# Kernel optimization log

Hardware: AMD Instinct MI355X
Metric: run time of the kernel (lower is better)

Reference implementation:

```python
import jax, jax.numpy as jnp
import numpy as np

B, H, S, D = 2, 16, 2048, 64
NUM_EMB = 8192  # 2 * max_position_embeddings


def setup_inputs() -> dict:
    key = jax.random.key(0)
    k1, k2, k3 = jax.random.split(key, 3)
    query = jax.random.normal(k1, (B, H, S, D), dtype=jnp.float32)
    attention_scores = jax.random.normal(k2, (B, H, S, S), dtype=jnp.float32)
    rel_emb = jax.random.normal(k3, (NUM_EMB, D), dtype=jnp.float32)
    return {"query": query, "attention_scores": attention_scores, "rel_emb": rel_emb}


def reference(query, attention_scores, rel_emb):
    seq_len = query.shape[2]
    pos = jnp.arange(seq_len)
    # relative ids in [0, 2*max_pos): (j - i) + num_embeddings // 2
    rel_ids = pos[None, :] - pos[:, None] + rel_emb.shape[0] // 2  # [S, S]
    bias = rel_emb[rel_ids]  # [S, S, D] gather (Toeplitz structure)
    # rel_logits[b,h,i,j] = sum_d query[b,h,i,d] * bias[i,j,d]
    rel_logits = jnp.einsum('bhid,ijd->bhij', query, bias)
    return attention_scores + rel_logits
```

## Files before the change

kernel.cpp:

```cpp
#include <hip/hip_runtime.h>

#define BH     32
#define S_LEN  2048
#define D_DIM  64
#define LDSTR  72

typedef _Float16 half8 __attribute__((ext_vector_type(8)));
typedef _Float16 half4 __attribute__((ext_vector_type(4)));
typedef float    f32x4 __attribute__((ext_vector_type(4)));

__global__ __launch_bounds__(256, 4)
void relpos_mfma_kernel(const float* __restrict__ q,
                        const float* __restrict__ sc,
                        const float* __restrict__ emb,
                        float* __restrict__ out)
{
    __shared__ _Float16 Alds[64  * LDSTR];
    __shared__ _Float16 Elds[128 * LDSTR];

    const int tid = threadIdx.x;
    int bid = blockIdx.x;
    const int tj = bid & 31;  bid >>= 5;
    const int ti = bid & 31;  bid >>= 5;
    const int bh = bid;
    const int i0 = ti * 64;
    const int j0 = tj * 64;
    const int rb = j0 - i0 + 4032;

    const float* qbase = q   + ((size_t)bh * S_LEN + i0) * D_DIM;
    const float* ebase = emb + (size_t)rb * D_DIM;
    #pragma unroll
    for (int k = 0; k < 4; ++k) {
        int f   = tid + k * 256;
        int row = f >> 4;
        int c4  = (f & 15) * 4;
        f32x4 v = *(const f32x4*)(qbase + row * D_DIM + c4);
        half4 h;
        h.x = (_Float16)v.x; h.y = (_Float16)v.y;
        h.z = (_Float16)v.z; h.w = (_Float16)v.w;
        *(half4*)&Alds[row * LDSTR + c4] = h;
    }
    #pragma unroll
    for (int k = 0; k < 8; ++k) {
        int f   = tid + k * 256;
        int row = f >> 4;
        int c4  = (f & 15) * 4;
        f32x4 v = *(const f32x4*)(ebase + row * D_DIM + c4);
        half4 h;
        h.x = (_Float16)v.x; h.y = (_Float16)v.y;
        h.z = (_Float16)v.z; h.w = (_Float16)v.w;
        *(half4*)&Elds[row * LDSTR + c4] = h;
    }
    __syncthreads();

    const int wave = tid >> 6;
    const int lane = tid & 63;
    const int lrow = lane & 15;
    const int quad = lane >> 4;
    const int ii_base = wave * 16 + quad * 4;

    const unsigned tbase = ((unsigned)(bh * S_LEN + i0)) * (unsigned)S_LEN + (unsigned)j0;
    f32x4 acc[2][4];
    #pragma unroll
    for (int h = 0; h < 2; ++h) {
        #pragma unroll
        for (int c = 0; c < 4; ++c) {
            int uu = c * 16 + lrow;
            #pragma unroll
            for (int r = 0; r < 4; ++r) {
                int ii = ii_base + r;
                int jj = ii + h * 64 + uu - 64;
                bool v = (unsigned)jj < 64u;
                acc[h][c][r] = v ? sc[tbase + (unsigned)(ii * S_LEN + jj)] : 0.0f;
            }
        }
    }

    const _Float16* arow = &Alds[(wave * 16 + lrow) * LDSTR + quad * 8];
    half8 a0 = *(const half8*)(arow);
    half8 a1 = *(const half8*)(arow + 32);

    #pragma unroll
    for (int h = 0; h < 2; ++h) {
        #pragma unroll
        for (int c = 0; c < 4; ++c) {
            const _Float16* brow = &Elds[(h * 64 + c * 16 + lrow) * LDSTR + quad * 8];
            half8 b0 = *(const half8*)(brow);
            half8 b1 = *(const half8*)(brow + 32);
            acc[h][c] = __builtin_amdgcn_mfma_f32_16x16x32_f16(a0, b0, acc[h][c], 0, 0, 0);
            acc[h][c] = __builtin_amdgcn_mfma_f32_16x16x32_f16(a1, b1, acc[h][c], 0, 0, 0);
        }
    }

    #pragma unroll
    for (int h = 0; h < 2; ++h) {
        #pragma unroll
        for (int c = 0; c < 4; ++c) {
            int uu = c * 16 + lrow;
            #pragma unroll
            for (int r = 0; r < 4; ++r) {
                int ii = ii_base + r;
                int jj = ii + h * 64 + uu - 64;
                if ((unsigned)jj < 64u) {
                    out[tbase + (unsigned)(ii * S_LEN + jj)] = acc[h][c][r];
                }
            }
        }
    }
}

extern "C" void kernel_launch(void* const* d_in, const int* in_sizes, int n_in,
                              void* d_out, int out_size, void* d_ws, size_t ws_size,
                              hipStream_t stream) {
    const float* q   = (const float*)d_in[0];
    const float* sc  = (const float*)d_in[1];
    const float* emb = (const float*)d_in[2];
    float* out = (float*)d_out;

    dim3 grid(BH * 32 * 32);
    relpos_mfma_kernel<<<grid, 256, 0, stream>>>(q, sc, emb, out);
}
```

Measured before the change: 1.022 ms.

## Give each block a full row strip, reusing Q and sliding embedding window

The kernel now launches one block per (bh, i-tile) and loops over all 32 j-tiles, instead of one block per 64x64 tile. Q fragments go straight into registers once per block. The embedding window is kept in a triple-buffered LDS ring so each 64-row chunk is loaded and converted once and reused by two adjacent j-tiles, with the next chunk prefetched during compute. This cuts redundant Q and embedding loads and LDS conversion. The cost is a grid of only 1024 blocks, which lowers parallelism and latency hiding on a memory-bound kernel.

```diff
diff --git a/kernel.cpp b/kernel.cpp
--- a/kernel.cpp
+++ b/kernel.cpp
@@ -1,6 +1,5 @@
 #include <hip/hip_runtime.h>
 
-#define BH     32
 #define S_LEN  2048
 #define D_DIM  64
 #define LDSTR  72
@@ -10,48 +9,17 @@
 typedef float    f32x4 __attribute__((ext_vector_type(4)));
 
 __global__ __launch_bounds__(256, 4)
-void relpos_mfma_kernel(const float* __restrict__ q,
-                        const float* __restrict__ sc,
-                        const float* __restrict__ emb,
-                        float* __restrict__ out)
+void relpos_row_kernel(const float* __restrict__ q,
+                       const float* __restrict__ sc,
+                       const float* __restrict__ emb,
+                       float* __restrict__ out)
 {
-    __shared__ _Float16 Alds[64  * LDSTR];
-    __shared__ _Float16 Elds[128 * LDSTR];
+    __shared__ _Float16 Elds[3][64 * LDSTR];
 
     const int tid = threadIdx.x;
-    int bid = blockIdx.x;
-    const int tj = bid & 31;  bid >>= 5;
-    const int ti = bid & 31;  bid >>= 5;
-    const int bh = bid;
-    const int i0 = ti * 64;
-    const int j0 = tj * 64;
-    const int rb = j0 - i0 + 4032;
-
-    const float* qbase = q   + ((size_t)bh * S_LEN + i0) * D_DIM;
-    const float* ebase = emb + (size_t)rb * D_DIM;
-    #pragma unroll
-    for (int k = 0; k < 4; ++k) {
-        int f   = tid + k * 256;
-        int row = f >> 4;
-        int c4  = (f & 15) * 4;
-        f32x4 v = *(const f32x4*)(qbase + row * D_DIM + c4);
-        half4 h;
-        h.x = (_Float16)v.x; h.y = (_Float16)v.y;
-        h.z = (_Float16)v.z; h.w = (_Float16)v.w;
-        *(half4*)&Alds[row * LDSTR + c4] = h;
-    }
-    #pragma unroll
-    for (int k = 0; k < 8; ++k) {
-        int f   = tid + k * 256;
-        int row = f >> 4;
-        int c4  = (f & 15) * 4;
-        f32x4 v = *(const f32x4*)(ebase + row * D_DIM + c4);
-        half4 h;
-        h.x = (_Float16)v.x; h.y = (_Float16)v.y;
-        h.z = (_Float16)v.z; h.w = (_Float16)v.w;
-        *(half4*)&Elds[row * LDSTR + c4] = h;
-    }
-    __syncthreads();
+    const int ti  = blockIdx.x & 31;
+    const int bh  = blockIdx.x >> 5;
+    const int i0  = ti * 64;
 
     const int wave = tid >> 6;
     const int lane = tid & 63;
@@ -59,53 +27,134 @@
     const int quad = lane >> 4;
     const int ii_base = wave * 16 + quad * 4;
 
-    const unsigned tbase = ((unsigned)(bh * S_LEN + i0)) * (unsigned)S_LEN + (unsigned)j0;
+    const int srow = tid >> 4;
+    const int scol = (tid & 15) * 4;
+
+    const float* embase = emb + (size_t)(4032 - i0) * D_DIM;
+
+    f32x4 er0[4], er1[4];
+    {
+        const float* e0 = embase;
+        const float* e1 = embase + 64 * D_DIM;
+        #pragma unroll
+        for (int k = 0; k < 4; ++k) {
+            er0[k] = *(const f32x4*)(e0 + (srow + k * 16) * D_DIM + scol);
+            er1[k] = *(const f32x4*)(e1 + (srow + k * 16) * D_DIM + scol);
+        }
+    }
+
+    half8 a0, a1;
+    {
+        const float* qrow = q + (size_t)(bh * S_LEN + i0 + wave * 16 + lrow) * D_DIM + quad * 8;
+        f32x4 v0 = *(const f32x4*)(qrow);
+        f32x4 v1 = *(const f32x4*)(qrow + 4);
+        f32x4 v2 = *(const f32x4*)(qrow + 32);
+        f32x4 v3 = *(const f32x4*)(qrow + 36);
+        a0[0] = (_Float16)v0.x; a0[1] = (_Float16)v0.y; a0[2] = (_Float16)v0.z; a0[3] = (_Float16)v0.w;
+        a0[4] = (_Float16)v1.x; a0[5] = (_Float16)v1.y; a0[6] = (_Float16)v1.z; a0[7] = (_Float16)v1.w;
+        a1[0] = (_Float16)v2.x; a1[1] = (_Float16)v2.y; a1[2] = (_Float16)v2.z; a1[3] = (_Float16)v2.w;
+        a1[4] = (_Float16)v3.x; a1[5] = (_Float16)v3.y; a1[6] = (_Float16)v3.z; a1[7] = (_Float16)v3.w;
+    }
+
+    const unsigned tb0 = ((unsigned)(bh * S_LEN + i0)) * (unsigned)S_LEN;
     f32x4 acc[2][4];
     #pragma unroll
     for (int h = 0; h < 2; ++h) {
         #pragma unroll
         for (int c = 0; c < 4; ++c) {
-            int uu = c * 16 + lrow;
+            const int uu = h * 64 + c * 16 + lrow;
             #pragma unroll
             for (int r = 0; r < 4; ++r) {
-                int ii = ii_base + r;
-                int jj = ii + h * 64 + uu - 64;
-                bool v = (unsigned)jj < 64u;
-                acc[h][c][r] = v ? sc[tbase + (unsigned)(ii * S_LEN + jj)] : 0.0f;
+                const int ii = ii_base + r;
+                const int jj = ii + uu - 64;
+                acc[h][c][r] = ((unsigned)jj < 64u)
+                             ? sc[tb0 + (unsigned)(ii * S_LEN + jj)] : 0.0f;
             }
         }
     }
 
-    const _Float16* arow = &Alds[(wave * 16 + lrow) * LDSTR + quad * 8];
-    half8 a0 = *(const half8*)(arow);
-    half8 a1 = *(const half8*)(arow + 32);
+    #pragma unroll
+    for (int k = 0; k < 4; ++k) {
+        half4 h0, h1;
+        h0.x = (_Float16)er0[k].x; h0.y = (_Float16)er0[k].y;
+        h0.z = (_Float16)er0[k].z; h0.w = (_Float16)er0[k].w;
+        h1.x = (_Float16)er1[k].x; h1.y = (_Float16)er1[k].y;
+        h1.z = (_Float16)er1[k].z; h1.w = (_Float16)er1[k].w;
+        *(half4*)&Elds[0][(srow + k * 16) * LDSTR + scol] = h0;
+        *(half4*)&Elds[1][(srow + k * 16) * LDSTR + scol] = h1;
+    }
+    __syncthreads();
 
-    #pragma unroll
-    for (int h = 0; h < 2; ++h) {
+    for (int tj = 0; tj < 32; ++tj) {
+        f32x4 er[4];
+        const bool pf = (tj <= 30);
+        if (pf) {
+            const float* en = embase + (size_t)(tj + 2) * 64 * D_DIM;
+            #pragma unroll
+            for (int k = 0; k < 4; ++k)
+                er[k] = *(const f32x4*)(en + (srow + k * 16) * D_DIM + scol);
+        }
+
+        const int s0 = tj % 3;
+        const int s1 = (tj + 1) % 3;
         #pragma unroll
-        for (int c = 0; c < 4; ++c) {
-            const _Float16* brow = &Elds[(h * 64 + c * 16 + lrow) * LDSTR + quad * 8];
-            half8 b0 = *(const half8*)(brow);
-            half8 b1 = *(const half8*)(brow + 32);
-            acc[h][c] = __builtin_amdgcn_mfma_f32_16x16x32_f16(a0, b0, acc[h][c], 0, 0, 0);
-            acc[h][c] = __builtin_amdgcn_mfma_f32_16x16x32_f16(a1, b1, acc[h][c], 0, 0, 0);
+        for (int h = 0; h < 2; ++h) {
+            const _Float16* bb = Elds[h ? s1 : s0];
+            #pragma unroll
+            for (int c = 0; c < 4; ++c) {
+                const _Float16* brow = bb + (c * 16 + lrow) * LDSTR + quad * 8;
+                half8 b0 = *(const half8*)(brow);
+                half8 b1 = *(const half8*)(brow + 32);
+                acc[h][c] = __builtin_amdgcn_mfma_f32_16x16x32_f16(a0, b0, acc[h][c], 0, 0, 0);
+                acc[h][c] = __builtin_amdgcn_mfma_f32_16x16x32_f16(a1, b1, acc[h][c], 0, 0, 0);
+            }
         }
-    }
 
-    #pragma unroll
-    for (int h = 0; h < 2; ++h) {
+        const unsigned tb = tb0 + (unsigned)(tj * 64);
         #pragma unroll
-        for (int c = 0; c < 4; ++c) {
-            int uu = c * 16 + lrow;
+        for (int h = 0; h < 2; ++h) {
             #pragma unroll
-            for (int r = 0; r < 4; ++r) {
-                int ii = ii_base + r;
-                int jj = ii + h * 64 + uu - 64;
-                if ((unsigned)jj < 64u) {
-                    out[tbase + (unsigned)(ii * S_LEN + jj)] = acc[h][c][r];
+            for (int c = 0; c < 4; ++c) {
+                const int uu = h * 64 + c * 16 + lrow;
+                #pragma unroll
+                for (int r = 0; r < 4; ++r) {
+                    const int ii = ii_base + r;
+                    const int jj = ii + uu - 64;
+                    if ((unsigned)jj < 64u)
+                        out[tb + (unsigned)(ii * S_LEN + jj)] = acc[h][c][r];
                 }
             }
         }
+
+        if (tj < 31) {
+            const unsigned tbn = tb + 64;
+            #pragma unroll
+            for (int h = 0; h < 2; ++h) {
+                #pragma unroll
+                for (int c = 0; c < 4; ++c) {
+                    const int uu = h * 64 + c * 16 + lrow;
+                    #pragma unroll
+                    for (int r = 0; r < 4; ++r) {
+                        const int ii = ii_base + r;
+                        const int jj = ii + uu - 64;
+                        acc[h][c][r] = ((unsigned)jj < 64u)
+                                     ? sc[tbn + (unsigned)(ii * S_LEN + jj)] : 0.0f;
+                    }
+                }
+            }
+        }
+
+        if (pf) {
+            _Float16* dst = Elds[(tj + 2) % 3];
+            #pragma unroll
+            for (int k = 0; k < 4; ++k) {
+                half4 hh;
+                hh.x = (_Float16)er[k].x; hh.y = (_Float16)er[k].y;
+                hh.z = (_Float16)er[k].z; hh.w = (_Float16)er[k].w;
+                *(half4*)&dst[(srow + k * 16) * LDSTR + scol] = hh;
+            }
+        }
+        __syncthreads();
     }
 }
 
@@ -117,6 +166,6 @@
     const float* emb = (const float*)d_in[2];
     float* out = (float*)d_out;
 
-    dim3 grid(BH * 32 * 32);
-    relpos_mfma_kernel<<<grid, 256, 0, stream>>>(q, sc, emb, out);
+    dim3 grid(32 * 32);
+    relpos_row_kernel<<<grid, 256, 0, stream>>>(q, sc, emb, out);
 }
```

New measurement: 962.8 us. -5.8%, faster.
